# Optimization experiments

Measured on AMD Instinct MI355X. Metric: run time of the kernel, lower is better.

Reference implementation:

```python
import jax, jax.numpy as jnp
import numpy as np

D_MODEL = 1024
NHEAD = 16
HEAD_DIM = D_MODEL // NHEAD
ROPE_BASE = 10000.0


def rope_cos_sin(seq_len, dim, dtype=jnp.float32):
    inv_freq = 1.0 / (ROPE_BASE ** (jnp.arange(0, dim, 2, dtype=jnp.float32) / dim))
    t = jnp.arange(seq_len, dtype=jnp.float32)
    freqs = jnp.einsum('i,j->ij', t, inv_freq)        # [S, dim/2]
    emb = jnp.concatenate([freqs, freqs], axis=-1)    # [S, dim]
    return emb.astype(dtype), jnp.cos(emb).astype(dtype), jnp.sin(emb).astype(dtype)


def rotate_half(x):
    x1, x2 = jnp.split(x, 2, axis=-1)
    return jnp.concatenate([-x2, x1], axis=-1)


def setup_inputs() -> dict:
    key = jax.random.key(0)
    ks = jax.random.split(key, 11)
    B, S, D = 2, 2048, D_MODEL
    std = 1.0 / np.sqrt(D)
    return {
        'query': jax.random.normal(ks[0], (B, S, D), jnp.float32),
        'key_': jax.random.normal(ks[1], (B, S, D), jnp.float32),
        'value': jax.random.normal(ks[2], (B, S, D), jnp.float32),
        'Wq': jax.random.uniform(ks[3], (D, D), jnp.float32, -std, std),
        'bq': jax.random.uniform(ks[4], (D,), jnp.float32, -std, std),
        'Wk': jax.random.uniform(ks[5], (D, D), jnp.float32, -std, std),
        'bk': jax.random.uniform(ks[6], (D,), jnp.float32, -std, std),
        'Wv': jax.random.uniform(ks[7], (D, D), jnp.float32, -std, std),
        'bv': jax.random.uniform(ks[8], (D,), jnp.float32, -std, std),
        'Wo': jax.random.uniform(ks[9], (D, D), jnp.float32, -std, std),
        'bo': jax.random.uniform(ks[10], (D,), jnp.float32, -std, std),
    }


def reference(query, key_, value, Wq, bq, Wk, bk, Wv, bv, Wo, bo):
    B, T, D = query.shape
    S = key_.shape[1]
    H, Hd = NHEAD, HEAD_DIM
    scale = Hd ** -0.5
    # projections (torch Linear: x @ W^T + b), reshape to [B, H, L, Hd]
    q = (query @ Wq.T + bq).reshape(B, T, H, Hd).transpose(0, 2, 1, 3)
    k = (key_ @ Wk.T + bk).reshape(B, S, H, Hd).transpose(0, 2, 1, 3)
    v = (value @ Wv.T + bv).reshape(B, S, H, Hd).transpose(0, 2, 1, 3)
    # RoPE
    _, cos, sin = rope_cos_sin(max(T, S), Hd, query.dtype)
    cos_q, sin_q = cos[:T][None, None], sin[:S][None, None]
    q = q * cos_q + rotate_half(q) * sin_q
    k = k * cos_q + rotate_half(k) * sin_q
    # attention
    scores = jnp.einsum('bhtd,bhsd->bhts', q, k) * scale
    attn = jax.nn.softmax(scores, axis=-1)
    out = jnp.einsum('bhts,bhsd->bhtd', attn, v)
    out = out.transpose(0, 2, 1, 3).reshape(B, T, D)
    return out @ Wo.T + bo
```

## Files before the change

kernel.cpp:

```cpp
#include <hip/hip_runtime.h>
#include <hip/hip_bf16.h>
#include <math.h>

using bf16x8 = __attribute__((ext_vector_type(8))) short;
using f32x4  = __attribute__((ext_vector_type(4))) float;

#define MFMA16(a,b,c) __builtin_amdgcn_mfma_f32_16x16x32_bf16(a,b,c,0,0,0)

#define GLOAD_LDS16(g, s) __builtin_amdgcn_global_load_lds( \
    (const __attribute__((address_space(1))) unsigned int*)(const void*)(g), \
    (__attribute__((address_space(3))) unsigned int*)(void*)(s), 16, 0, 0)

static __device__ __forceinline__ short f2bf(float f) {
    __hip_bfloat16 h = __float2bfloat16(f);
    return *reinterpret_cast<short*>(&h);
}

__global__ void prep_cast(const float* q, const float* k, const float* v,
                          const float* wq, const float* wk, const float* wv, const float* wo,
                          short* xq, short* xk, short* xv,
                          short* bwq, short* bwk, short* bwv, short* bwo) {
    const long NBIG = 1L << 20;
    const long NW   = 1L << 18;
    const long total = 3*NBIG + 4*NW;
    for (long i = (long)blockIdx.x*blockDim.x + threadIdx.x; i < total; i += (long)gridDim.x*blockDim.x) {
        const float* src; short* dst; long j = i;
        if (j < NBIG)              { src = q;  dst = xq;  }
        else if ((j -= NBIG) < NBIG) { src = k;  dst = xk;  }
        else if ((j -= NBIG) < NBIG) { src = v;  dst = xv;  }
        else if ((j -= NBIG) < NW)   { src = wq; dst = bwq; }
        else if ((j -= NW) < NW)     { src = wk; dst = bwk; }
        else if ((j -= NW) < NW)     { src = wv; dst = bwv; }
        else { j -= NW;              src = wo; dst = bwo; }
        float4 f = reinterpret_cast<const float4*>(src)[j];
        ushort4 o;
        o.x = (ushort)f2bf(f.x); o.y = (ushort)f2bf(f.y);
        o.z = (ushort)f2bf(f.z); o.w = (ushort)f2bf(f.w);
        reinterpret_cast<ushort4*>(dst)[j] = o;
    }
}

__global__ void rope_table(float* cost, float* sint) {
    int i = blockIdx.x*blockDim.x + threadIdx.x;
    int s = i >> 5, j = i & 31;
    double inv = pow(10000.0, -(double)j / 32.0);
    double a = (double)s * inv;
    cost[i] = (float)cos(a);
    sint[i] = (float)sin(a);
}

__device__ __forceinline__ void gemm_tile(const short* A, const short* B,
                                          int brow, int bcol, f32x4 (&acc)[4][4]) {
    __shared__ __align__(16) short Al[2][128*32];
    __shared__ __align__(16) short Bl[2][128*32];
    const int t = threadIdx.x;
    const int l = t & 63, qi = l & 15, h = l >> 4;
    const int w = t >> 6, wr = w >> 1, wc = w & 1;
    const f32x4 z4 = {0.f, 0.f, 0.f, 0.f};
#pragma unroll
    for (int i = 0; i < 4; ++i)
#pragma unroll
        for (int j = 0; j < 4; ++j) acc[i][j] = z4;

    const int srow = w*32 + (l >> 2);
    const int scol = (l & 3) << 3;
    const short* ga = A + (long)(brow + srow)*1024 + scol;
    const short* gb = B + (long)(bcol + srow)*1024 + scol;
    const int lo = w*32*32;

    GLOAD_LDS16(ga,            Al[0] + lo);
    GLOAD_LDS16(ga + 16*1024,  Al[0] + lo + 16*32);
    GLOAD_LDS16(gb,            Bl[0] + lo);
    GLOAD_LDS16(gb + 16*1024,  Bl[0] + lo + 16*32);
    asm volatile("s_waitcnt vmcnt(0)");
    __syncthreads();

    int cur = 0;
    for (int kt = 0; kt < 32; ++kt) {
        if (kt < 31) {
            int nb = cur ^ 1;
            GLOAD_LDS16(ga + ((kt+1) << 5),            Al[nb] + lo);
            GLOAD_LDS16(ga + ((kt+1) << 5) + 16*1024,  Al[nb] + lo + 16*32);
            GLOAD_LDS16(gb + ((kt+1) << 5),            Bl[nb] + lo);
            GLOAD_LDS16(gb + ((kt+1) << 5) + 16*1024,  Bl[nb] + lo + 16*32);
        }
        bf16x8 af[4], bfr[4];
#pragma unroll
        for (int mf = 0; mf < 4; ++mf)
            af[mf] = *(const bf16x8*)(Al[cur] + (wr*64 + mf*16 + qi)*32 + h*8);
#pragma unroll
        for (int nf = 0; nf < 4; ++nf)
            bfr[nf] = *(const bf16x8*)(Bl[cur] + (wc*64 + nf*16 + qi)*32 + h*8);
        __builtin_amdgcn_s_setprio(1);
#pragma unroll
        for (int mf = 0; mf < 4; ++mf)
#pragma unroll
            for (int nf = 0; nf < 4; ++nf)
                acc[mf][nf] = MFMA16(af[mf], bfr[nf], acc[mf][nf]);
        __builtin_amdgcn_s_setprio(0);
        asm volatile("s_waitcnt vmcnt(0)");
        __syncthreads();
        cur ^= 1;
    }
}

__global__ __launch_bounds__(256, 3)
void gemm_qkv_kernel(const short* xq, const short* xk, const short* xv,
                     const short* wq, const short* wk, const short* wv,
                     const float* biq, const float* bik, const float* biv,
                     short* qo, short* ko, short* vo,
                     const float* cost, const float* sint) {
    const int mode = blockIdx.z;
    const short* A    = mode == 0 ? xq  : (mode == 1 ? xk  : xv);
    const short* B    = mode == 0 ? wq  : (mode == 1 ? wk  : wv);
    const float* bias = mode == 0 ? biq : (mode == 1 ? bik : biv);
    const int brow = blockIdx.x * 128, bcol = blockIdx.y * 128;
    f32x4 acc[4][4];
    gemm_tile(A, B, brow, bcol, acc);

    const int t = threadIdx.x;
    const int l = t & 63, qi = l & 15, h = l >> 4;
    const int w = t >> 6, wr = w >> 1, wc = w & 1;
    const int n0 = bcol + wc*64, m0 = brow + wr*64;

    if (mode < 2) {
        short* dst = mode == 0 ? qo : ko;
        const float sc = (mode == 0) ? 0.125f : 1.0f;
#pragma unroll
        for (int nf = 0; nf < 2; ++nf) {
            const int j = nf*16 + qi;
            const float b0 = bias[n0 + nf*16 + qi];
            const float b1 = bias[n0 + (nf+2)*16 + qi];
#pragma unroll
            for (int mf = 0; mf < 4; ++mf) {
#pragma unroll
                for (int r = 0; r < 4; ++r) {
                    int m = m0 + mf*16 + 4*h + r;
                    int s = m & 2047;
                    float c  = cost[s*32 + j];
                    float si = sint[s*32 + j];
                    float x0 = acc[mf][nf  ][r] + b0;
                    float x1 = acc[mf][nf+2][r] + b1;
                    dst[(long)m*1024 + n0 + nf*16 + qi]      = f2bf((x0*c - x1*si) * sc);
                    dst[(long)m*1024 + n0 + (nf+2)*16 + qi]  = f2bf((x1*c + x0*si) * sc);
                }
            }
        }
    } else {
#pragma unroll
        for (int mf = 0; mf < 4; ++mf) {
#pragma unroll
            for (int nf = 0; nf < 4; ++nf) {
                int col = n0 + nf*16 + qi;
                float bb = bias[col];
                int mbase = m0 + mf*16 + 4*h;
                int bb_  = mbase >> 11, s0 = mbase & 2047;
                int hh = col >> 6, d = col & 63;
                ushort4 pk;
                pk.x = (ushort)f2bf(acc[mf][nf][0] + bb);
                pk.y = (ushort)f2bf(acc[mf][nf][1] + bb);
                pk.z = (ushort)f2bf(acc[mf][nf][2] + bb);
                pk.w = (ushort)f2bf(acc[mf][nf][3] + bb);
                *(ushort4*)(vo + (long)((bb_*16 + hh)*64 + d)*2048 + s0) = pk;
            }
        }
    }
}

__global__ __launch_bounds__(256, 3)
void gemm_o_kernel(const short* A, const short* B, const float* bias, float* out) {
    const int brow = blockIdx.x * 128, bcol = blockIdx.y * 128;
    f32x4 acc[4][4];
    gemm_tile(A, B, brow, bcol, acc);
    const int t = threadIdx.x;
    const int l = t & 63, qi = l & 15, h = l >> 4;
    const int w = t >> 6, wr = w >> 1, wc = w & 1;
    const int n0 = bcol + wc*64, m0 = brow + wr*64;
#pragma unroll
    for (int nf = 0; nf < 4; ++nf) {
        float bb = bias[n0 + nf*16 + qi];
#pragma unroll
        for (int mf = 0; mf < 4; ++mf) {
#pragma unroll
            for (int r = 0; r < 4; ++r) {
                int m = m0 + mf*16 + 4*h + r;
                out[(long)m*1024 + n0 + nf*16 + qi] = acc[mf][nf][r] + bb;
            }
        }
    }
}

__global__ __launch_bounds__(256, 2)
void attn_kernel(const short* qw, const short* kw, const short* vtw, short* ow) {
    __shared__ __align__(16) short Kl[64*64];
    __shared__ __align__(16) short Vl[64*64];
    __shared__ __align__(16) short Pl[4][32*64];
    const int t = threadIdx.x;
    const int w = t >> 6, l = t & 63, qi = l & 15, h = l >> 4;
    const int b = blockIdx.z, hh = blockIdx.y;
    const long qrow0 = (long)b*2048 + blockIdx.x*128 + w*32;
    short* myP = &Pl[w][0];

    bf16x8 bqf[2][2];
#pragma unroll
    for (int nf = 0; nf < 2; ++nf)
#pragma unroll
        for (int kf = 0; kf < 2; ++kf)
            bqf[nf][kf] = *(const bf16x8*)(qw + (qrow0 + nf*16 + qi)*1024 + hh*64 + kf*32 + h*8);

    const f32x4 z4 = {0.f, 0.f, 0.f, 0.f};
    f32x4 o[2][4];
#pragma unroll
    for (int mi = 0; mi < 2; ++mi)
#pragma unroll
        for (int nd = 0; nd < 4; ++nd) o[mi][nd] = z4;
    float mrun[2] = {-INFINITY, -INFINITY};
    float lrun[2] = {0.f, 0.f};

    const short* Kg = kw  + (long)b*2048*1024 + hh*64;
    const short* Vg = vtw + (long)(b*16 + hh)*64*2048;

    for (int jt = 0; jt < 32; ++jt) {
        __syncthreads();
#pragma unroll
        for (int cc = 0; cc < 2; ++cc) {
            int c  = t + (cc << 8);
            int r0 = c >> 3, e0 = (c & 7) << 3;
            int4 kv = *(const int4*)(Kg + (long)(jt*64 + r0)*1024 + e0);
            int4 vv = *(const int4*)(Vg + (long)r0*2048 + jt*64 + e0);
            *(int4*)((char*)Kl + (((r0*64 + e0)*2) ^ ((r0 & 7) << 4))) = kv;
            *(int4*)((char*)Vl + (((r0*64 + e0)*2) ^ ((r0 & 7) << 4))) = vv;
        }
        __syncthreads();

        f32x4 sc[4][2];
#pragma unroll
        for (int mf = 0; mf < 4; ++mf) { sc[mf][0] = z4; sc[mf][1] = z4; }
        __builtin_amdgcn_s_setprio(1);
#pragma unroll
        for (int kf = 0; kf < 2; ++kf) {
#pragma unroll
            for (int mf = 0; mf < 4; ++mf) {
                bf16x8 ka = *(const bf16x8*)((char*)Kl +
                    ((((mf*16 + qi)*64 + kf*32 + h*8)*2) ^ ((qi & 7) << 4)));
                sc[mf][0] = MFMA16(ka, bqf[0][kf], sc[mf][0]);
                sc[mf][1] = MFMA16(ka, bqf[1][kf], sc[mf][1]);
            }
        }
        __builtin_amdgcn_s_setprio(0);

        float csc[2];
#pragma unroll
        for (int nf = 0; nf < 2; ++nf) {
            float tm = -INFINITY;
#pragma unroll
            for (int mf = 0; mf < 4; ++mf)
#pragma unroll
                for (int r = 0; r < 4; ++r) tm = fmaxf(tm, sc[mf][nf][r]);
            tm = fmaxf(tm, __shfl_xor(tm, 16));
            tm = fmaxf(tm, __shfl_xor(tm, 32));
            float mnew = fmaxf(mrun[nf], tm);
            float corr = __expf(mrun[nf] - mnew);
            float ts = 0.f;
#pragma unroll
            for (int mf = 0; mf < 4; ++mf) {
                float p0 = __expf(sc[mf][nf][0] - mnew);
                float p1 = __expf(sc[mf][nf][1] - mnew);
                float p2 = __expf(sc[mf][nf][2] - mnew);
                float p3 = __expf(sc[mf][nf][3] - mnew);
                ts += p0 + p1 + p2 + p3;
                ushort4 pk;
                pk.x = (ushort)f2bf(p0); pk.y = (ushort)f2bf(p1);
                pk.z = (ushort)f2bf(p2); pk.w = (ushort)f2bf(p3);
                *(ushort4*)((char*)myP +
                    ((((nf*16 + qi)*64 + mf*16 + 4*h)*2) ^ ((qi & 7) << 4))) = pk;
            }
            ts += __shfl_xor(ts, 16);
            ts += __shfl_xor(ts, 32);
            lrun[nf] = lrun[nf]*corr + ts;
            mrun[nf] = mnew;
            csc[nf] = corr;
        }

#pragma unroll
        for (int mi = 0; mi < 2; ++mi)
#pragma unroll
            for (int r = 0; r < 4; ++r) {
                float f = __shfl(csc[mi], 4*h + r);
#pragma unroll
                for (int nd = 0; nd < 4; ++nd) o[mi][nd][r] *= f;
            }

        __builtin_amdgcn_s_setprio(1);
#pragma unroll
        for (int kf = 0; kf < 2; ++kf) {
            bf16x8 pa[2], vb[4];
#pragma unroll
            for (int mi = 0; mi < 2; ++mi)
                pa[mi] = *(const bf16x8*)((char*)myP +
                    ((((mi*16 + qi)*64 + kf*32 + h*8)*2) ^ ((qi & 7) << 4)));
#pragma unroll
            for (int nd = 0; nd < 4; ++nd)
                vb[nd] = *(const bf16x8*)((char*)Vl +
                    ((((nd*16 + qi)*64 + kf*32 + h*8)*2) ^ ((qi & 7) << 4)));
#pragma unroll
            for (int mi = 0; mi < 2; ++mi)
#pragma unroll
                for (int nd = 0; nd < 4; ++nd)
                    o[mi][nd] = MFMA16(pa[mi], vb[nd], o[mi][nd]);
        }
        __builtin_amdgcn_s_setprio(0);
    }

    float rinv[2] = {1.f/lrun[0], 1.f/lrun[1]};
#pragma unroll
    for (int mi = 0; mi < 2; ++mi)
#pragma unroll
        for (int r = 0; r < 4; ++r) {
            float f = __shfl(rinv[mi], 4*h + r);
#pragma unroll
            for (int nd = 0; nd < 4; ++nd)
                ow[(qrow0 + mi*16 + 4*h + r)*1024 + hh*64 + nd*16 + qi] =
                    f2bf(o[mi][nd][r] * f);
        }
}

extern "C" void kernel_launch(void* const* d_in, const int* in_sizes, int n_in,
                              void* d_out, int out_size, void* d_ws, size_t ws_size,
                              hipStream_t stream) {
    const float* query = (const float*)d_in[0];
    const float* key_  = (const float*)d_in[1];
    const float* value = (const float*)d_in[2];
    const float* Wq = (const float*)d_in[3];
    const float* bq = (const float*)d_in[4];
    const float* Wk = (const float*)d_in[5];
    const float* bk = (const float*)d_in[6];
    const float* Wv = (const float*)d_in[7];
    const float* bv = (const float*)d_in[8];
    const float* Wo = (const float*)d_in[9];
    const float* bo = (const float*)d_in[10];
    float* out = (float*)d_out;

    char* ws = (char*)d_ws;
    const size_t MB = 1u << 20;
    short* xq  = (short*)(ws);
    short* xk  = (short*)(ws + 8*MB);
    short* xv  = (short*)(ws + 16*MB);
    short* wqb = (short*)(ws + 24*MB);
    short* wkb = (short*)(ws + 26*MB);
    short* wvb = (short*)(ws + 28*MB);
    short* wob = (short*)(ws + 30*MB);
    short* qws = (short*)(ws + 32*MB);
    short* kws = (short*)(ws + 40*MB);
    short* vtw = (short*)(ws + 48*MB);
    float* cost = (float*)(ws + 56*MB);
    float* sint = (float*)(ws + 56*MB + 2048*32*4);
    short* attn = xq;

    hipLaunchKernelGGL(prep_cast, dim3(2048), dim3(256), 0, stream,
                       query, key_, value, Wq, Wk, Wv, Wo,
                       xq, xk, xv, wqb, wkb, wvb, wob);
    hipLaunchKernelGGL(rope_table, dim3(256), dim3(256), 0, stream, cost, sint);
    hipLaunchKernelGGL(gemm_qkv_kernel, dim3(32, 8, 3), dim3(256), 0, stream,
                       xq, xk, xv, wqb, wkb, wvb, bq, bk, bv,
                       qws, kws, vtw, cost, sint);
    hipLaunchKernelGGL(attn_kernel, dim3(16, 16, 2), dim3(256), 0, stream,
                       qws, kws, vtw, attn);
    hipLaunchKernelGGL(gemm_o_kernel, dim3(32, 8), dim3(256), 0, stream,
                       attn, wob, bo, out);
}
```

Measured before the change: 246.3 us.

## Use 32x32 MFMA in attention with register-resident P and LDS-staged V transpose

The attention kernel moves from 16x16x32 MFMAs to 32x32x16 MFMAs, giving each lane one query row. Softmax probabilities are packed to bf16 with v_cvt_pk_bf16_f32 and exchanged across lanes with shuffles instead of going through an LDS P buffer. Row max and sum reductions shrink to a single cross-half shuffle. Separately, the V projection epilogue now stages its transpose through shared LDS (the GEMM's LDS is made explicit so it can be reused) and writes coalesced 16-byte stores instead of scattered 8-byte stores. The trade-off is larger accumulator register pressure and more complex lane-exchange logic.

```diff
diff --git a/kernel.cpp b/kernel.cpp
--- a/kernel.cpp
+++ b/kernel.cpp
@@ -4,8 +4,10 @@
 
 using bf16x8 = __attribute__((ext_vector_type(8))) short;
 using f32x4  = __attribute__((ext_vector_type(4))) float;
+using f32x16 = __attribute__((ext_vector_type(16))) float;
 
 #define MFMA16(a,b,c) __builtin_amdgcn_mfma_f32_16x16x32_bf16(a,b,c,0,0,0)
+#define MFMA32(a,b,c) __builtin_amdgcn_mfma_f32_32x32x16_bf16(a,b,c,0,0,0)
 
 #define GLOAD_LDS16(g, s) __builtin_amdgcn_global_load_lds( \
     (const __attribute__((address_space(1))) unsigned int*)(const void*)(g), \
@@ -14,6 +16,12 @@
 static __device__ __forceinline__ short f2bf(float f) {
     __hip_bfloat16 h = __float2bfloat16(f);
     return *reinterpret_cast<short*>(&h);
+}
+
+static __device__ __forceinline__ int cvtpk(float lo, float hi) {
+    int r;
+    asm volatile("v_cvt_pk_bf16_f32 %0, %1, %2" : "=v"(r) : "v"(lo), "v"(hi));
+    return r;
 }
 
 __global__ void prep_cast(const float* q, const float* k, const float* v,
@@ -50,9 +58,12 @@
 }
 
 __device__ __forceinline__ void gemm_tile(const short* A, const short* B,
-                                          int brow, int bcol, f32x4 (&acc)[4][4]) {
-    __shared__ __align__(16) short Al[2][128*32];
-    __shared__ __align__(16) short Bl[2][128*32];
+                                          int brow, int bcol, short* lds,
+                                          f32x4 (&acc)[4][4]) {
+    short* Al0 = lds;
+    short* Al1 = lds + 4096;
+    short* Bl0 = lds + 8192;
+    short* Bl1 = lds + 12288;
     const int t = threadIdx.x;
     const int l = t & 63, qi = l & 15, h = l >> 4;
     const int w = t >> 6, wr = w >> 1, wc = w & 1;
@@ -68,29 +79,32 @@
     const short* gb = B + (long)(bcol + srow)*1024 + scol;
     const int lo = w*32*32;
 
-    GLOAD_LDS16(ga,            Al[0] + lo);
-    GLOAD_LDS16(ga + 16*1024,  Al[0] + lo + 16*32);
-    GLOAD_LDS16(gb,            Bl[0] + lo);
-    GLOAD_LDS16(gb + 16*1024,  Bl[0] + lo + 16*32);
+    GLOAD_LDS16(ga,            Al0 + lo);
+    GLOAD_LDS16(ga + 16*1024,  Al0 + lo + 16*32);
+    GLOAD_LDS16(gb,            Bl0 + lo);
+    GLOAD_LDS16(gb + 16*1024,  Bl0 + lo + 16*32);
     asm volatile("s_waitcnt vmcnt(0)");
     __syncthreads();
 
     int cur = 0;
     for (int kt = 0; kt < 32; ++kt) {
         if (kt < 31) {
-            int nb = cur ^ 1;
-            GLOAD_LDS16(ga + ((kt+1) << 5),            Al[nb] + lo);
-            GLOAD_LDS16(ga + ((kt+1) << 5) + 16*1024,  Al[nb] + lo + 16*32);
-            GLOAD_LDS16(gb + ((kt+1) << 5),            Bl[nb] + lo);
-            GLOAD_LDS16(gb + ((kt+1) << 5) + 16*1024,  Bl[nb] + lo + 16*32);
-        }
+            short* An = cur ? Al0 : Al1;
+            short* Bn = cur ? Bl0 : Bl1;
+            GLOAD_LDS16(ga + ((kt+1) << 5),            An + lo);
+            GLOAD_LDS16(ga + ((kt+1) << 5) + 16*1024,  An + lo + 16*32);
+            GLOAD_LDS16(gb + ((kt+1) << 5),            Bn + lo);
+            GLOAD_LDS16(gb + ((kt+1) << 5) + 16*1024,  Bn + lo + 16*32);
+        }
+        const short* Ac = cur ? Al1 : Al0;
+        const short* Bc = cur ? Bl1 : Bl0;
         bf16x8 af[4], bfr[4];
 #pragma unroll
         for (int mf = 0; mf < 4; ++mf)
-            af[mf] = *(const bf16x8*)(Al[cur] + (wr*64 + mf*16 + qi)*32 + h*8);
+            af[mf] = *(const bf16x8*)(Ac + (wr*64 + mf*16 + qi)*32 + h*8);
 #pragma unroll
         for (int nf = 0; nf < 4; ++nf)
-            bfr[nf] = *(const bf16x8*)(Bl[cur] + (wc*64 + nf*16 + qi)*32 + h*8);
+            bfr[nf] = *(const bf16x8*)(Bc + (wc*64 + nf*16 + qi)*32 + h*8);
         __builtin_amdgcn_s_setprio(1);
 #pragma unroll
         for (int mf = 0; mf < 4; ++mf)
@@ -110,13 +124,14 @@
                      const float* biq, const float* bik, const float* biv,
                      short* qo, short* ko, short* vo,
                      const float* cost, const float* sint) {
+    __shared__ __align__(16) short lds[16384];
     const int mode = blockIdx.z;
     const short* A    = mode == 0 ? xq  : (mode == 1 ? xk  : xv);
     const short* B    = mode == 0 ? wq  : (mode == 1 ? wk  : wv);
     const float* bias = mode == 0 ? biq : (mode == 1 ? bik : biv);
     const int brow = blockIdx.x * 128, bcol = blockIdx.y * 128;
     f32x4 acc[4][4];
-    gemm_tile(A, B, brow, bcol, acc);
+    gemm_tile(A, B, brow, bcol, lds, acc);
 
     const int t = threadIdx.x;
     const int l = t & 63, qi = l & 15, h = l >> 4;
@@ -147,31 +162,41 @@
             }
         }
     } else {
-#pragma unroll
-        for (int mf = 0; mf < 4; ++mf) {
-#pragma unroll
-            for (int nf = 0; nf < 4; ++nf) {
-                int col = n0 + nf*16 + qi;
-                float bb = bias[col];
-                int mbase = m0 + mf*16 + 4*h;
-                int bb_  = mbase >> 11, s0 = mbase & 2047;
-                int hh = col >> 6, d = col & 63;
-                ushort4 pk;
-                pk.x = (ushort)f2bf(acc[mf][nf][0] + bb);
-                pk.y = (ushort)f2bf(acc[mf][nf][1] + bb);
-                pk.z = (ushort)f2bf(acc[mf][nf][2] + bb);
-                pk.w = (ushort)f2bf(acc[mf][nf][3] + bb);
-                *(ushort4*)(vo + (long)((bb_*16 + hh)*64 + d)*2048 + s0) = pk;
-            }
+        __syncthreads();
+        short* tb = lds + w*4096;
+#pragma unroll
+        for (int nf = 0; nf < 4; ++nf) {
+            const int dl = nf*16 + qi;
+            const float bb = bias[n0 + dl];
+#pragma unroll
+            for (int mf = 0; mf < 4; ++mf) {
+#pragma unroll
+                for (int r = 0; r < 4; ++r) {
+                    const int sl = mf*16 + 4*h + r;
+                    *(short*)((char*)tb + (((dl*64 + sl)*2) ^ ((dl & 7) << 4))) =
+                        f2bf(acc[mf][nf][r] + bb);
+                }
+            }
+        }
+        const int hh2 = n0 >> 6;
+        const int bb2 = m0 >> 11;
+        const long s0g = (long)(m0 & 2047);
+#pragma unroll
+        for (int i = 0; i < 8; ++i) {
+            const int c = l + (i << 6);
+            const int dl = c >> 3, so = (c & 7) << 3;
+            int4 vv = *(const int4*)((char*)tb + (((dl*64 + so)*2) ^ ((dl & 7) << 4)));
+            *(int4*)(vo + (long)((bb2*16 + hh2)*64 + dl)*2048 + s0g + so) = vv;
         }
     }
 }
 
 __global__ __launch_bounds__(256, 3)
 void gemm_o_kernel(const short* A, const short* B, const float* bias, float* out) {
+    __shared__ __align__(16) short lds[16384];
     const int brow = blockIdx.x * 128, bcol = blockIdx.y * 128;
     f32x4 acc[4][4];
-    gemm_tile(A, B, brow, bcol, acc);
+    gemm_tile(A, B, brow, bcol, lds, acc);
     const int t = threadIdx.x;
     const int l = t & 63, qi = l & 15, h = l >> 4;
     const int w = t >> 6, wr = w >> 1, wc = w & 1;
@@ -194,135 +219,131 @@
 void attn_kernel(const short* qw, const short* kw, const short* vtw, short* ow) {
     __shared__ __align__(16) short Kl[64*64];
     __shared__ __align__(16) short Vl[64*64];
-    __shared__ __align__(16) short Pl[4][32*64];
     const int t = threadIdx.x;
-    const int w = t >> 6, l = t & 63, qi = l & 15, h = l >> 4;
+    const int w = t >> 6, l = t & 63;
+    const int q5 = l & 31, hi = l >> 5;
     const int b = blockIdx.z, hh = blockIdx.y;
-    const long qrow0 = (long)b*2048 + blockIdx.x*128 + w*32;
-    short* myP = &Pl[w][0];
-
-    bf16x8 bqf[2][2];
-#pragma unroll
-    for (int nf = 0; nf < 2; ++nf)
-#pragma unroll
-        for (int kf = 0; kf < 2; ++kf)
-            bqf[nf][kf] = *(const bf16x8*)(qw + (qrow0 + nf*16 + qi)*1024 + hh*64 + kf*32 + h*8);
-
-    const f32x4 z4 = {0.f, 0.f, 0.f, 0.f};
-    f32x4 o[2][4];
-#pragma unroll
-    for (int mi = 0; mi < 2; ++mi)
-#pragma unroll
-        for (int nd = 0; nd < 4; ++nd) o[mi][nd] = z4;
-    float mrun[2] = {-INFINITY, -INFINITY};
-    float lrun[2] = {0.f, 0.f};
+    const long qrow = (long)b*2048 + blockIdx.x*128 + w*32 + q5;
+
+    bf16x8 bqf[4];
+#pragma unroll
+    for (int s = 0; s < 4; ++s)
+        bqf[s] = *(const bf16x8*)(qw + qrow*1024 + hh*64 + s*16 + hi*8);
+
+    f32x16 o0, o1;
+#pragma unroll
+    for (int r = 0; r < 16; ++r) { o0[r] = 0.f; o1[r] = 0.f; }
+    float mrun = -INFINITY, lrun = 0.f;
 
     const short* Kg = kw  + (long)b*2048*1024 + hh*64;
     const short* Vg = vtw + (long)(b*16 + hh)*64*2048;
 
+    const int r0a = t >> 3,        e0a = (t & 7) << 3;
+    const int r0b = (t+256) >> 3,  e0b = ((t+256) & 7) << 3;
+
     for (int jt = 0; jt < 32; ++jt) {
         __syncthreads();
-#pragma unroll
-        for (int cc = 0; cc < 2; ++cc) {
-            int c  = t + (cc << 8);
-            int r0 = c >> 3, e0 = (c & 7) << 3;
-            int4 kv = *(const int4*)(Kg + (long)(jt*64 + r0)*1024 + e0);
-            int4 vv = *(const int4*)(Vg + (long)r0*2048 + jt*64 + e0);
-            *(int4*)((char*)Kl + (((r0*64 + e0)*2) ^ ((r0 & 7) << 4))) = kv;
-            *(int4*)((char*)Vl + (((r0*64 + e0)*2) ^ ((r0 & 7) << 4))) = vv;
+        {
+            int4 ka = *(const int4*)(Kg + (long)(jt*64 + r0a)*1024 + e0a);
+            int4 va = *(const int4*)(Vg + (long)r0a*2048 + jt*64 + e0a);
+            int4 kb = *(const int4*)(Kg + (long)(jt*64 + r0b)*1024 + e0b);
+            int4 vb = *(const int4*)(Vg + (long)r0b*2048 + jt*64 + e0b);
+            *(int4*)((char*)Kl + (((r0a*64 + e0a)*2) ^ ((r0a & 7) << 4))) = ka;
+            *(int4*)((char*)Vl + (((r0a*64 + e0a)*2) ^ ((r0a & 7) << 4))) = va;
+            *(int4*)((char*)Kl + (((r0b*64 + e0b)*2) ^ ((r0b & 7) << 4))) = kb;
+            *(int4*)((char*)Vl + (((r0b*64 + e0b)*2) ^ ((r0b & 7) << 4))) = vb;
         }
         __syncthreads();
 
-        f32x4 sc[4][2];
-#pragma unroll
-        for (int mf = 0; mf < 4; ++mf) { sc[mf][0] = z4; sc[mf][1] = z4; }
+        f32x16 s0v, s1v;
+#pragma unroll
+        for (int r = 0; r < 16; ++r) { s0v[r] = 0.f; s1v[r] = 0.f; }
         __builtin_amdgcn_s_setprio(1);
 #pragma unroll
-        for (int kf = 0; kf < 2; ++kf) {
-#pragma unroll
-            for (int mf = 0; mf < 4; ++mf) {
-                bf16x8 ka = *(const bf16x8*)((char*)Kl +
-                    ((((mf*16 + qi)*64 + kf*32 + h*8)*2) ^ ((qi & 7) << 4)));
-                sc[mf][0] = MFMA16(ka, bqf[0][kf], sc[mf][0]);
-                sc[mf][1] = MFMA16(ka, bqf[1][kf], sc[mf][1]);
-            }
+        for (int s = 0; s < 4; ++s) {
+            const int cb = (s*16 + hi*8) * 2;
+            bf16x8 ka0 = *(const bf16x8*)((char*)Kl + (((q5*64*2) + cb) ^ ((q5 & 7) << 4)));
+            bf16x8 ka1 = *(const bf16x8*)((char*)Kl + ((((32+q5)*64*2) + cb) ^ ((q5 & 7) << 4)));
+            s0v = MFMA32(ka0, bqf[s], s0v);
+            s1v = MFMA32(ka1, bqf[s], s1v);
         }
         __builtin_amdgcn_s_setprio(0);
 
-        float csc[2];
-#pragma unroll
-        for (int nf = 0; nf < 2; ++nf) {
-            float tm = -INFINITY;
-#pragma unroll
-            for (int mf = 0; mf < 4; ++mf)
-#pragma unroll
-                for (int r = 0; r < 4; ++r) tm = fmaxf(tm, sc[mf][nf][r]);
-            tm = fmaxf(tm, __shfl_xor(tm, 16));
-            tm = fmaxf(tm, __shfl_xor(tm, 32));
-            float mnew = fmaxf(mrun[nf], tm);
-            float corr = __expf(mrun[nf] - mnew);
-            float ts = 0.f;
-#pragma unroll
-            for (int mf = 0; mf < 4; ++mf) {
-                float p0 = __expf(sc[mf][nf][0] - mnew);
-                float p1 = __expf(sc[mf][nf][1] - mnew);
-                float p2 = __expf(sc[mf][nf][2] - mnew);
-                float p3 = __expf(sc[mf][nf][3] - mnew);
-                ts += p0 + p1 + p2 + p3;
-                ushort4 pk;
-                pk.x = (ushort)f2bf(p0); pk.y = (ushort)f2bf(p1);
-                pk.z = (ushort)f2bf(p2); pk.w = (ushort)f2bf(p3);
-                *(ushort4*)((char*)myP +
-                    ((((nf*16 + qi)*64 + mf*16 + 4*h)*2) ^ ((qi & 7) << 4))) = pk;
-            }
-            ts += __shfl_xor(ts, 16);
-            ts += __shfl_xor(ts, 32);
-            lrun[nf] = lrun[nf]*corr + ts;
-            mrun[nf] = mnew;
-            csc[nf] = corr;
-        }
-
-#pragma unroll
-        for (int mi = 0; mi < 2; ++mi)
-#pragma unroll
-            for (int r = 0; r < 4; ++r) {
-                float f = __shfl(csc[mi], 4*h + r);
-#pragma unroll
-                for (int nd = 0; nd < 4; ++nd) o[mi][nd][r] *= f;
-            }
+        float tm = -INFINITY;
+#pragma unroll
+        for (int r = 0; r < 16; ++r) { tm = fmaxf(tm, s0v[r]); tm = fmaxf(tm, s1v[r]); }
+        tm = fmaxf(tm, __shfl_xor(tm, 32));
+        const float mnew = fmaxf(mrun, tm);
+        const float corr = __expf(mrun - mnew);
+        float ts = 0.f;
+#pragma unroll
+        for (int r = 0; r < 16; ++r) {
+            s0v[r] = __expf(s0v[r] - mnew);
+            s1v[r] = __expf(s1v[r] - mnew);
+            ts += s0v[r] + s1v[r];
+        }
+        ts += __shfl_xor(ts, 32);
+        lrun = lrun*corr + ts;
+        mrun = mnew;
+#pragma unroll
+        for (int r = 0; r < 16; ++r) { o0[r] *= corr; o1[r] *= corr; }
+
+        bf16x8 pf[4];
+#pragma unroll
+        for (int tt = 0; tt < 2; ++tt) {
+#pragma unroll
+            for (int ss = 0; ss < 2; ++ss) {
+                const int base = 8*ss;
+                float p0, p1, p2, p3, p4, p5, p6, p7;
+                if (tt == 0) {
+                    p0=s0v[base+0]; p1=s0v[base+1]; p2=s0v[base+2]; p3=s0v[base+3];
+                    p4=s0v[base+4]; p5=s0v[base+5]; p6=s0v[base+6]; p7=s0v[base+7];
+                } else {
+                    p0=s1v[base+0]; p1=s1v[base+1]; p2=s1v[base+2]; p3=s1v[base+3];
+                    p4=s1v[base+4]; p5=s1v[base+5]; p6=s1v[base+6]; p7=s1v[base+7];
+                }
+                int X0 = cvtpk(p0, p1), Y0 = cvtpk(p2, p3);
+                int X1 = cvtpk(p4, p5), Y1 = cvtpk(p6, p7);
+                int sx0 = __shfl_xor(X0, 32), sy0 = __shfl_xor(Y0, 32);
+                int sx1 = __shfl_xor(X1, 32), sy1 = __shfl_xor(Y1, 32);
+                union { int i[4]; bf16x8 v; } u;
+                u.i[0] = hi ? sx1 : X0;
+                u.i[1] = hi ? sy1 : Y0;
+                u.i[2] = hi ? X1  : sx0;
+                u.i[3] = hi ? Y1  : sy0;
+                pf[2*tt + ss] = u.v;
+            }
+        }
 
         __builtin_amdgcn_s_setprio(1);
 #pragma unroll
-        for (int kf = 0; kf < 2; ++kf) {
-            bf16x8 pa[2], vb[4];
-#pragma unroll
-            for (int mi = 0; mi < 2; ++mi)
-                pa[mi] = *(const bf16x8*)((char*)myP +
-                    ((((mi*16 + qi)*64 + kf*32 + h*8)*2) ^ ((qi & 7) << 4)));
-#pragma unroll
-            for (int nd = 0; nd < 4; ++nd)
-                vb[nd] = *(const bf16x8*)((char*)Vl +
-                    ((((nd*16 + qi)*64 + kf*32 + h*8)*2) ^ ((qi & 7) << 4)));
-#pragma unroll
-            for (int mi = 0; mi < 2; ++mi)
-#pragma unroll
-                for (int nd = 0; nd < 4; ++nd)
-                    o[mi][nd] = MFMA16(pa[mi], vb[nd], o[mi][nd]);
+        for (int s4 = 0; s4 < 4; ++s4) {
+            const int cb = (s4*16 + hi*8) * 2;
+            bf16x8 va0 = *(const bf16x8*)((char*)Vl + (((q5*64*2) + cb) ^ ((q5 & 7) << 4)));
+            bf16x8 va1 = *(const bf16x8*)((char*)Vl + ((((32+q5)*64*2) + cb) ^ ((q5 & 7) << 4)));
+            o0 = MFMA32(va0, pf[s4], o0);
+            o1 = MFMA32(va1, pf[s4], o1);
         }
         __builtin_amdgcn_s_setprio(0);
     }
 
-    float rinv[2] = {1.f/lrun[0], 1.f/lrun[1]};
-#pragma unroll
-    for (int mi = 0; mi < 2; ++mi)
-#pragma unroll
-        for (int r = 0; r < 4; ++r) {
-            float f = __shfl(rinv[mi], 4*h + r);
-#pragma unroll
-            for (int nd = 0; nd < 4; ++nd)
-                ow[(qrow0 + mi*16 + 4*h + r)*1024 + hh*64 + nd*16 + qi] =
-                    f2bf(o[mi][nd][r] * f);
-        }
+    const float inv = 1.f / lrun;
+    const long obase = qrow*1024 + hh*64;
+#pragma unroll
+    for (int dt = 0; dt < 2; ++dt) {
+#pragma unroll
+        for (int j = 0; j < 4; ++j) {
+            ushort4 pk;
+            if (dt == 0) {
+                pk.x = (ushort)f2bf(o0[4*j+0]*inv); pk.y = (ushort)f2bf(o0[4*j+1]*inv);
+                pk.z = (ushort)f2bf(o0[4*j+2]*inv); pk.w = (ushort)f2bf(o0[4*j+3]*inv);
+            } else {
+                pk.x = (ushort)f2bf(o1[4*j+0]*inv); pk.y = (ushort)f2bf(o1[4*j+1]*inv);
+                pk.z = (ushort)f2bf(o1[4*j+2]*inv); pk.w = (ushort)f2bf(o1[4*j+3]*inv);
+            }
+            *(ushort4*)(ow + obase + dt*32 + 8*j + 4*hi) = pk;
+        }
+    }
 }
 
 extern "C" void kernel_launch(void* const* d_in, const int* in_sizes, int n_in,
```

New measurement: 238.6 us. 3.1% less time.
